# Kernel tuning notes

Hardware: AMD Instinct MI355X
Metric: run time of the kernel (lower is better)

Reference implementation:

```python
import jax, jax.numpy as jnp
import numpy as np

B, N, X, Y, W1, W2, D = 2, 6, 8, 8, 8, 8, 128
H, DH = 4, 32
L = X * Y          # number of windows
QT = N * W1 * W2   # tokens per window
EPS = 1e-5


def _ln(x, g, b):
    m = x.mean(-1, keepdims=True)
    v = ((x - m) ** 2).mean(-1, keepdims=True)
    return (x - m) * jax.lax.rsqrt(v + EPS) * g + b


def _win(t):
    # b n x y w1 w2 d -> b (x y) (n w1 w2) d
    return t.transpose(0, 2, 3, 1, 4, 5, 6).reshape(B, L, QT, D)


def setup_inputs() -> dict:
    key = jax.random.key(0)
    ks = jax.random.split(key, 12)
    s = 0.02
    inp = {
        'q': jax.random.normal(ks[0], (B, N, X, Y, W1, W2, D), jnp.float32),
        'k': jax.random.normal(ks[1], (B, N, X, Y, W1, W2, D), jnp.float32),
        'v': jax.random.normal(ks[2], (B, N, X, Y, W1, W2, D), jnp.float32),
        'skip': jax.random.normal(ks[3], (B, X, Y, W1, W2, D), jnp.float32),
        'gq': jnp.ones((D,), jnp.float32), 'betq': jnp.zeros((D,), jnp.float32),
        'gk': jnp.ones((D,), jnp.float32), 'betk': jnp.zeros((D,), jnp.float32),
        'gv': jnp.ones((D,), jnp.float32), 'betv': jnp.zeros((D,), jnp.float32),
        'wq': jax.random.normal(ks[4], (D, H * DH), jnp.float32) * s,
        'bq': jnp.zeros((H * DH,), jnp.float32),
        'wk': jax.random.normal(ks[5], (D, H * DH), jnp.float32) * s,
        'bk': jnp.zeros((H * DH,), jnp.float32),
        'wv': jax.random.normal(ks[6], (D, H * DH), jnp.float32) * s,
        'bv': jnp.zeros((H * DH,), jnp.float32),
        'wp': jax.random.normal(ks[7], (H * DH, D), jnp.float32) * s,
        'bp': jnp.zeros((D,), jnp.float32),
    }
    return inp


def reference(q, k, v, skip, gq, betq, gk, betk, gv, betv,
              wq, bq, wk, bk, wv, bv, wp, bp):
    scale = DH ** -0.5
    qw, kw, vw = _win(q), _win(k), _win(v)
    # LayerNorm + Linear QKV, split heads: (b, l, T, h, dh)
    qh = (_ln(qw, gq, betq) @ wq + bq).reshape(B, L, QT, H, DH)
    kh = (_ln(kw, gk, betk) @ wk + bk).reshape(B, L, QT, H, DH)
    vh = (_ln(vw, gv, betv) @ wv + bv).reshape(B, L, QT, H, DH)
    dot = scale * jnp.einsum('blqhd,blkhd->bhlqk', qh, kh)
    att = jax.nn.softmax(dot, axis=-1)
    a = jnp.einsum('bhlqk,blkhd->blqhd', att, vh).reshape(B, L, QT, H * DH)
    # b (x y) (n w1 w2) d -> b n x y w1 w2 d
    a = a.reshape(B, X, Y, N, W1, W2, H * DH).transpose(0, 3, 1, 2, 4, 5, 6)
    z = a @ wp + bp
    z = z.mean(1)  # average over views
    return z + skip
```

## Files before the change

kernel.cpp:

```cpp
#include <hip/hip_runtime.h>


typedef unsigned short u16;
typedef __bf16 bf16x8 __attribute__((ext_vector_type(8)));
typedef float  f32x16 __attribute__((ext_vector_type(16)));
typedef unsigned short u16x8 __attribute__((ext_vector_type(8)));

__device__ __forceinline__ u16 f2bf(float f){
  unsigned u = __float_as_uint(f);
  u += 0x7fffu + ((u >> 16) & 1u);
  return (u16)(u >> 16);
}

__device__ __forceinline__ f32x16 mfma_bf16(bf16x8 a, bf16x8 b, f32x16 c){
  return __builtin_amdgcn_mfma_f32_32x32x16_bf16(a, b, c, 0, 0, 0);
}


__global__ __launch_bounds__(128) void k_prep(
    const float* __restrict__ wq, const float* __restrict__ bq,
    const float* __restrict__ gq, const float* __restrict__ betq,
    const float* __restrict__ wk, const float* __restrict__ bk,
    const float* __restrict__ gk, const float* __restrict__ betk,
    const float* __restrict__ wv, const float* __restrict__ bv,
    const float* __restrict__ gv, const float* __restrict__ betv,
    const float* __restrict__ wp,
    u16* __restrict__ wqT, u16* __restrict__ wkT, u16* __restrict__ wvT, u16* __restrict__ wpT,
    float* __restrict__ bq2, float* __restrict__ bk2, float* __restrict__ bv2)
{
  const float ALPHA_Q = 0.17677669529663687f * 1.4426950408889634f;
  int wsel = blockIdx.x >> 2, qq = blockIdx.x & 3;
  int tid = threadIdx.x;
  const float *w, *bb, *g, *bet; u16* wT; float* b2; float alpha;
  if (wsel == 0){ w=wq; bb=bq; g=gq; bet=betq; wT=wqT; b2=bq2; alpha=ALPHA_Q; }
  else if (wsel == 1){ w=wk; bb=bk; g=gk; bet=betk; wT=wkT; b2=bk2; alpha=1.f; }
  else if (wsel == 2){ w=wv; bb=bv; g=gv; bet=betv; wT=wvT; b2=bv2; alpha=1.f; }
  else { w=wp; bb=nullptr; g=nullptr; bet=nullptr; wT=wpT; b2=nullptr; alpha=1.f; }
  float sc = (g ? g[tid] : 1.f) * alpha;
  for (int nn = 0; nn < 32; nn++){
    int n = qq*32 + nn;
    wT[n*128 + tid] = f2bf(w[tid*128 + n] * sc);
  }
  if (qq == 0 && bb){
    float s = bb[tid];
    for (int k2 = 0; k2 < 128; k2++) s += bet[k2] * w[k2*128 + tid];
    b2[tid] = s * alpha;
  }
}

__global__ __launch_bounds__(256) void k_lnproj(
    const float* __restrict__ qg, const float* __restrict__ kg, const float* __restrict__ vg,
    const u16* __restrict__ wqT, const u16* __restrict__ wkT, const u16* __restrict__ wvT,
    const float* __restrict__ bq2, const float* __restrict__ bk2, const float* __restrict__ bv2,
    u16* __restrict__ qh, u16* __restrict__ kh, u16* __restrict__ vh)
{
  __shared__ alignas(16) float Af[64*132];
  __shared__ float mean_s[64], rstd_s[64];
  __shared__ alignas(16) u16 Abf[64*136];
  int bid = blockIdx.x, tid = threadIdx.x;
  int which = bid % 3;
  int t = bid / 3;
  int n = t % 6, bl = t / 6;
  const float* src; const u16* wT; const float* b2; u16* dstb;
  if (which == 0){ src=qg; wT=wqT; b2=bq2; dstb=qh; }
  else if (which == 1){ src=kg; wT=wkT; b2=bk2; dstb=kh; }
  else { src=vg; wT=wvT; b2=bv2; dstb=vh; }
  int b = bl >> 6, l = bl & 63;
  const float4* s4 = (const float4*)(src + (size_t)((b*6 + n)*64 + l)*64*128);
  #pragma unroll
  for (int i = 0; i < 8; i++){
    int idx = tid + i*256;
    int row = idx >> 5, c4 = idx & 31;
    *(float4*)&Af[row*132 + c4*4] = s4[row*32 + c4];
  }
  __syncthreads();
  if (tid < 64){
    float s = 0.f, s2 = 0.f;
    for (int i = 0; i < 128; i++){
      int d = ((tid & 31) + i) & 127;
      float x = Af[tid*132 + d];
      s += x; s2 += x*x;
    }
    float m = s * (1.f/128.f);
    mean_s[tid] = m;
    rstd_s[tid] = rsqrtf(s2*(1.f/128.f) - m*m + 1e-5f);
  }
  __syncthreads();
  #pragma unroll
  for (int i = 0; i < 32; i++){
    int idx = tid + i*256;
    int row = idx >> 7, d = idx & 127;
    Abf[row*136 + d] = f2bf((Af[row*132 + d] - mean_s[row]) * rstd_s[row]);
  }
  __syncthreads();
  int wave = tid >> 6, lane = tid & 63, lm = lane & 31, lh = lane >> 5;
  bf16x8 bfr[8];
  const u16* wrow = wT + (32*wave + lm)*128 + lh*8;
  #pragma unroll
  for (int ks = 0; ks < 8; ks++) bfr[ks] = *(const bf16x8*)(wrow + ks*16);
  f32x16 acc0, acc1;
  #pragma unroll
  for (int r = 0; r < 16; r++){ acc0[r]=0.f; acc1[r]=0.f; }
  #pragma unroll
  for (int ks = 0; ks < 8; ks++){
    bf16x8 a0 = *(const bf16x8*)&Abf[lm*136       + ks*16 + lh*8];
    bf16x8 a1 = *(const bf16x8*)&Abf[(32+lm)*136  + ks*16 + lh*8];
    acc0 = mfma_bf16(a0, bfr[ks], acc0);
    acc1 = mfma_bf16(a1, bfr[ks], acc1);
  }
  float bias = b2[32*wave + lm];
  u16* dst = dstb + ((size_t)(bl*4 + wave)*384 + n*64)*32 + lm;
  #pragma unroll
  for (int r = 0; r < 16; r++){
    int row0 = (r&3) + 8*(r>>2) + 4*lh;
    dst[(size_t)row0*32]      = f2bf(acc0[r] + bias);
    dst[(size_t)(32+row0)*32] = f2bf(acc1[r] + bias);
  }
}

__global__ __launch_bounds__(384) void k_attn(
    const u16* __restrict__ qh, const u16* __restrict__ kh, const u16* __restrict__ vh,
    u16* __restrict__ abar)
{
  __shared__ alignas(16) u16 vts[32*392];
  __shared__ alignas(16) u16 ps[6*32*40];
  __shared__ float abar_s[64*32];
  int bid = blockIdx.x, tid = threadIdx.x;
  int h = bid & 3, bl = bid >> 2;
  const u16* qb = qh + (size_t)bid * (384*32);
  const u16* kb = kh + (size_t)bid * (384*32);
  const u16* vb = vh + (size_t)bid * (384*32);

  #pragma unroll
  for (int i = 0; i < 4; i++){
    int c = tid + i*384;
    int row = c >> 2, part = c & 3;
    u16x8 vv = *(const u16x8*)(vb + row*32 + part*8);
    #pragma unroll
    for (int j = 0; j < 8; j++) vts[(part*8 + j)*392 + row] = vv[j];
  }
  for (int idx = tid; idx < 2048; idx += 384) abar_s[idx] = 0.f;
  __syncthreads();

  int wave = tid >> 6, lane = tid & 63, lm = lane & 31, lh = lane >> 5;
  u16* pw = &ps[wave * (32*40)];

  bf16x8 qf[2][2];
  #pragma unroll
  for (int rt = 0; rt < 2; rt++)
    #pragma unroll
    for (int ks = 0; ks < 2; ks++)
      qf[rt][ks] = *(const bf16x8*)(qb + (wave*64 + rt*32 + lm)*32 + ks*16 + lh*8);

  f32x16 oacc[2];
  float lsum[32];
  #pragma unroll
  for (int r = 0; r < 16; r++){ oacc[0][r] = 0.f; oacc[1][r] = 0.f; }
  #pragma unroll
  for (int r = 0; r < 32; r++) lsum[r] = 0.f;

  for (int kt = 0; kt < 12; kt++){
    int K0 = kt*32;
    bf16x8 kf0 = *(const bf16x8*)(kb + (K0+lm)*32 +      lh*8);
    bf16x8 kf1 = *(const bf16x8*)(kb + (K0+lm)*32 + 16 + lh*8);
    bf16x8 vf0 = *(const bf16x8*)&vts[lm*392 + K0 +      lh*8];
    bf16x8 vf1 = *(const bf16x8*)&vts[lm*392 + K0 + 16 + lh*8];
    #pragma unroll
    for (int rt = 0; rt < 2; rt++){
      f32x16 s;
      #pragma unroll
      for (int r = 0; r < 16; r++) s[r] = 0.f;
      s = mfma_bf16(qf[rt][0], kf0, s);
      s = mfma_bf16(qf[rt][1], kf1, s);
      #pragma unroll
      for (int r = 0; r < 16; r++){
        float e = exp2f(s[r]);
        lsum[rt*16 + r] += e;
        pw[((r&3) + 8*(r>>2) + 4*lh)*40 + lm] = f2bf(e);
      }
      bf16x8 pf0 = *(const bf16x8*)&pw[lm*40 +      lh*8];
      bf16x8 pf1 = *(const bf16x8*)&pw[lm*40 + 16 + lh*8];
      oacc[rt] = mfma_bf16(pf0, vf0, oacc[rt]);
      oacc[rt] = mfma_bf16(pf1, vf1, oacc[rt]);
    }
  }

  #pragma unroll
  for (int rt = 0; rt < 2; rt++){
    #pragma unroll
    for (int r = 0; r < 16; r++){
      float sle = lsum[rt*16 + r];
      #pragma unroll
      for (int m = 1; m < 32; m <<= 1) sle += __shfl_xor(sle, m, 64);
      float o = oacc[rt][r] * ((1.f/6.f) / sle);
      int row0 = (r&3) + 8*(r>>2) + 4*lh;
      atomicAdd(&abar_s[(rt*32 + row0)*32 + lm], o);
    }
  }
  __syncthreads();
  u16* ob = abar + (size_t)(bl*64)*128 + h*32;
  for (int idx = tid; idx < 2048; idx += 384){
    int w12 = idx >> 5, dh = idx & 31;
    ob[(size_t)w12*128 + dh] = f2bf(abar_s[idx]);
  }
}

__global__ __launch_bounds__(256) void k_out(
    const u16* __restrict__ abar, const u16* __restrict__ wpT,
    const float* __restrict__ bp, const float* __restrict__ skip,
    float* __restrict__ out)
{
  __shared__ alignas(16) u16 Als[64*136];
  int tid = threadIdx.x;
  int R0 = blockIdx.x * 64;
  #pragma unroll
  for (int i = 0; i < 4; i++){
    int c = tid + i*256;
    int row = c >> 4, part = c & 15;
    *(u16x8*)&Als[row*136 + part*8] = *(const u16x8*)(abar + (size_t)(R0+row)*128 + part*8);
  }
  __syncthreads();
  int wave = tid >> 6, lane = tid & 63, lm = lane & 31, lh = lane >> 5;
  bf16x8 bfr[8];
  const u16* wrow = wpT + (32*wave + lm)*128 + lh*8;
  #pragma unroll
  for (int ks = 0; ks < 8; ks++) bfr[ks] = *(const bf16x8*)(wrow + ks*16);
  f32x16 acc0, acc1;
  #pragma unroll
  for (int r = 0; r < 16; r++){ acc0[r]=0.f; acc1[r]=0.f; }
  #pragma unroll
  for (int ks = 0; ks < 8; ks++){
    bf16x8 a0 = *(const bf16x8*)&Als[lm*136      + ks*16 + lh*8];
    bf16x8 a1 = *(const bf16x8*)&Als[(32+lm)*136 + ks*16 + lh*8];
    acc0 = mfma_bf16(a0, bfr[ks], acc0);
    acc1 = mfma_bf16(a1, bfr[ks], acc1);
  }
  float bias = bp[32*wave + lm];
  #pragma unroll
  for (int r = 0; r < 16; r++){
    int row0 = (r&3) + 8*(r>>2) + 4*lh;
    size_t f0 = (size_t)(R0 + row0)*128 + 32*wave + lm;
    out[f0] = acc0[r] + bias + skip[f0];
    size_t f1 = (size_t)(R0 + 32 + row0)*128 + 32*wave + lm;
    out[f1] = acc1[r] + bias + skip[f1];
  }
}

extern "C" void kernel_launch(void* const* d_in, const int* in_sizes, int n_in,
                              void* d_out, int out_size, void* d_ws, size_t ws_size,
                              hipStream_t stream)
{
  const float* q    = (const float*)d_in[0];
  const float* k    = (const float*)d_in[1];
  const float* v    = (const float*)d_in[2];
  const float* skip = (const float*)d_in[3];
  const float* gq   = (const float*)d_in[4];
  const float* betq = (const float*)d_in[5];
  const float* gk   = (const float*)d_in[6];
  const float* betk = (const float*)d_in[7];
  const float* gv   = (const float*)d_in[8];
  const float* betv = (const float*)d_in[9];
  const float* wq   = (const float*)d_in[10];
  const float* bq   = (const float*)d_in[11];
  const float* wk   = (const float*)d_in[12];
  const float* bk   = (const float*)d_in[13];
  const float* wv   = (const float*)d_in[14];
  const float* bv   = (const float*)d_in[15];
  const float* wp   = (const float*)d_in[16];
  const float* bp   = (const float*)d_in[17];
  float* out = (float*)d_out;

  char* ws = (char*)d_ws;
  u16* wqT = (u16*)ws;
  u16* wkT = wqT + 16384;
  u16* wvT = wkT + 16384;
  u16* wpT = wvT + 16384;
  float* bq2 = (float*)(ws + 131072);
  float* bk2 = bq2 + 128;
  float* bv2 = bk2 + 128;
  u16* qh = (u16*)(ws + 132608);
  u16* kh = qh + 6291456;
  u16* vh = kh + 6291456;
  u16* abar = vh + 6291456;

  k_prep  <<<16,   128, 0, stream>>>(wq,bq,gq,betq, wk,bk,gk,betk, wv,bv,gv,betv, wp,
                                     wqT,wkT,wvT,wpT, bq2,bk2,bv2);
  k_lnproj<<<2304, 256, 0, stream>>>(q,k,v, wqT,wkT,wvT, bq2,bk2,bv2, qh,kh,vh);
  k_attn  <<<512,  384, 0, stream>>>(qh,kh,vh, abar);
  k_out   <<<128,  256, 0, stream>>>(abar, wpT, bp, skip, out);
}
```

Baseline: 230.1 us.

## Fold LayerNorm into GEMM epilogue and keep softmax probabilities in registers

The LN+projection kernel now computes row sums with wave shuffles while loading, converts raw inputs straight to bf16, and applies mean/rstd after the MFMA through precomputed per-column sums of gamma-scaled weights. This removes the fp32 staging tile, one LDS pass and a barrier. The attention kernel swaps the operand order so each lane's P fragment can be fed directly into the PV MFMA, with V keys permuted in LDS to match. That drops the per-wave P round trip through shared memory, and the kernel now runs 12 waves of one 32-row tile each. Applying normalization after a bf16 GEMM on unnormalized inputs loses some precision when row means are large.

```diff
diff --git a/kernel.cpp b/kernel.cpp
--- a/kernel.cpp
+++ b/kernel.cpp
@@ -5,6 +5,9 @@
 typedef __bf16 bf16x8 __attribute__((ext_vector_type(8)));
 typedef float  f32x16 __attribute__((ext_vector_type(16)));
 typedef unsigned short u16x8 __attribute__((ext_vector_type(8)));
+typedef unsigned short u16x4 __attribute__((ext_vector_type(4)));
+
+union U8 { u16x8 u; bf16x8 b; };
 
 __device__ __forceinline__ u16 f2bf(float f){
   unsigned u = __float_as_uint(f);
@@ -26,25 +29,31 @@
     const float* __restrict__ gv, const float* __restrict__ betv,
     const float* __restrict__ wp,
     u16* __restrict__ wqT, u16* __restrict__ wkT, u16* __restrict__ wvT, u16* __restrict__ wpT,
-    float* __restrict__ bq2, float* __restrict__ bk2, float* __restrict__ bv2)
+    float* __restrict__ bq2, float* __restrict__ bk2, float* __restrict__ bv2,
+    float* __restrict__ uq2, float* __restrict__ uk2, float* __restrict__ uv2)
 {
   const float ALPHA_Q = 0.17677669529663687f * 1.4426950408889634f;
   int wsel = blockIdx.x >> 2, qq = blockIdx.x & 3;
   int tid = threadIdx.x;
-  const float *w, *bb, *g, *bet; u16* wT; float* b2; float alpha;
-  if (wsel == 0){ w=wq; bb=bq; g=gq; bet=betq; wT=wqT; b2=bq2; alpha=ALPHA_Q; }
-  else if (wsel == 1){ w=wk; bb=bk; g=gk; bet=betk; wT=wkT; b2=bk2; alpha=1.f; }
-  else if (wsel == 2){ w=wv; bb=bv; g=gv; bet=betv; wT=wvT; b2=bv2; alpha=1.f; }
-  else { w=wp; bb=nullptr; g=nullptr; bet=nullptr; wT=wpT; b2=nullptr; alpha=1.f; }
+  const float *w, *bb, *g, *bet; u16* wT; float *b2, *u2; float alpha;
+  if (wsel == 0){ w=wq; bb=bq; g=gq; bet=betq; wT=wqT; b2=bq2; u2=uq2; alpha=ALPHA_Q; }
+  else if (wsel == 1){ w=wk; bb=bk; g=gk; bet=betk; wT=wkT; b2=bk2; u2=uk2; alpha=1.f; }
+  else if (wsel == 2){ w=wv; bb=bv; g=gv; bet=betv; wT=wvT; b2=bv2; u2=uv2; alpha=1.f; }
+  else { w=wp; bb=nullptr; g=nullptr; bet=nullptr; wT=wpT; b2=nullptr; u2=nullptr; alpha=1.f; }
   float sc = (g ? g[tid] : 1.f) * alpha;
   for (int nn = 0; nn < 32; nn++){
     int n = qq*32 + nn;
     wT[n*128 + tid] = f2bf(w[tid*128 + n] * sc);
   }
   if (qq == 0 && bb){
-    float s = bb[tid];
-    for (int k2 = 0; k2 < 128; k2++) s += bet[k2] * w[k2*128 + tid];
+    float s = bb[tid], su = 0.f;
+    for (int k2 = 0; k2 < 128; k2++){
+      float wv_ = w[k2*128 + tid];
+      s  += bet[k2] * wv_;
+      su += g[k2] * wv_;
+    }
     b2[tid] = s * alpha;
+    u2[tid] = su * alpha;
   }
 }
 
@@ -52,47 +61,44 @@
     const float* __restrict__ qg, const float* __restrict__ kg, const float* __restrict__ vg,
     const u16* __restrict__ wqT, const u16* __restrict__ wkT, const u16* __restrict__ wvT,
     const float* __restrict__ bq2, const float* __restrict__ bk2, const float* __restrict__ bv2,
+    const float* __restrict__ uq2, const float* __restrict__ uk2, const float* __restrict__ uv2,
     u16* __restrict__ qh, u16* __restrict__ kh, u16* __restrict__ vh)
 {
-  __shared__ alignas(16) float Af[64*132];
-  __shared__ float mean_s[64], rstd_s[64];
   __shared__ alignas(16) u16 Abf[64*136];
+  __shared__ float s1s[64], s2s[64];
   int bid = blockIdx.x, tid = threadIdx.x;
   int which = bid % 3;
   int t = bid / 3;
   int n = t % 6, bl = t / 6;
-  const float* src; const u16* wT; const float* b2; u16* dstb;
-  if (which == 0){ src=qg; wT=wqT; b2=bq2; dstb=qh; }
-  else if (which == 1){ src=kg; wT=wkT; b2=bk2; dstb=kh; }
-  else { src=vg; wT=wvT; b2=bv2; dstb=vh; }
+  const float* src; const u16* wT; const float *b2, *u2; u16* dstb;
+  if (which == 0){ src=qg; wT=wqT; b2=bq2; u2=uq2; dstb=qh; }
+  else if (which == 1){ src=kg; wT=wkT; b2=bk2; u2=uk2; dstb=kh; }
+  else { src=vg; wT=wvT; b2=bv2; u2=uv2; dstb=vh; }
   int b = bl >> 6, l = bl & 63;
   const float4* s4 = (const float4*)(src + (size_t)((b*6 + n)*64 + l)*64*128);
   #pragma unroll
   for (int i = 0; i < 8; i++){
     int idx = tid + i*256;
     int row = idx >> 5, c4 = idx & 31;
-    *(float4*)&Af[row*132 + c4*4] = s4[row*32 + c4];
+    float4 xv = s4[idx];
+    float s1 = xv.x + xv.y + xv.z + xv.w;
+    float s2 = xv.x*xv.x + xv.y*xv.y + xv.z*xv.z + xv.w*xv.w;
+    #pragma unroll
+    for (int m = 1; m < 32; m <<= 1){
+      s1 += __shfl_xor(s1, m, 64);
+      s2 += __shfl_xor(s2, m, 64);
+    }
+    if (c4 == 0){ s1s[row] = s1; s2s[row] = s2; }
+    u16x4 pk = { f2bf(xv.x), f2bf(xv.y), f2bf(xv.z), f2bf(xv.w) };
+    *(u16x4*)&Abf[row*136 + c4*4] = pk;
   }
   __syncthreads();
   if (tid < 64){
-    float s = 0.f, s2 = 0.f;
-    for (int i = 0; i < 128; i++){
-      int d = ((tid & 31) + i) & 127;
-      float x = Af[tid*132 + d];
-      s += x; s2 += x*x;
-    }
-    float m = s * (1.f/128.f);
-    mean_s[tid] = m;
-    rstd_s[tid] = rsqrtf(s2*(1.f/128.f) - m*m + 1e-5f);
-  }
-  __syncthreads();
-  #pragma unroll
-  for (int i = 0; i < 32; i++){
-    int idx = tid + i*256;
-    int row = idx >> 7, d = idx & 127;
-    Abf[row*136 + d] = f2bf((Af[row*132 + d] - mean_s[row]) * rstd_s[row]);
-  }
-  __syncthreads();
+    float m = s1s[tid] * (1.f/128.f);
+    float r = rsqrtf(s2s[tid] * (1.f/128.f) - m*m + 1e-5f);
+    s1s[tid] = r;
+    s2s[tid] = r * m;
+  }
   int wave = tid >> 6, lane = tid & 63, lm = lane & 31, lh = lane >> 5;
   bf16x8 bfr[8];
   const u16* wrow = wT + (32*wave + lm)*128 + lh*8;
@@ -108,22 +114,25 @@
     acc0 = mfma_bf16(a0, bfr[ks], acc0);
     acc1 = mfma_bf16(a1, bfr[ks], acc1);
   }
-  float bias = b2[32*wave + lm];
+  __syncthreads();
+  int col = 32*wave + lm;
+  float u2c = u2[col], bc = b2[col];
   u16* dst = dstb + ((size_t)(bl*4 + wave)*384 + n*64)*32 + lm;
   #pragma unroll
   for (int r = 0; r < 16; r++){
     int row0 = (r&3) + 8*(r>>2) + 4*lh;
-    dst[(size_t)row0*32]      = f2bf(acc0[r] + bias);
-    dst[(size_t)(32+row0)*32] = f2bf(acc1[r] + bias);
-  }
-}
-
-__global__ __launch_bounds__(384) void k_attn(
+    float y0 = s1s[row0]     * acc0[r] - s2s[row0]     * u2c + bc;
+    float y1 = s1s[row0+32]  * acc1[r] - s2s[row0+32]  * u2c + bc;
+    dst[(size_t)row0*32]      = f2bf(y0);
+    dst[(size_t)(32+row0)*32] = f2bf(y1);
+  }
+}
+
+__global__ __launch_bounds__(768, 6) void k_attn(
     const u16* __restrict__ qh, const u16* __restrict__ kh, const u16* __restrict__ vh,
     u16* __restrict__ abar)
 {
-  __shared__ alignas(16) u16 vts[32*392];
-  __shared__ alignas(16) u16 ps[6*32*40];
+  __shared__ alignas(16) u16 vts[32*408];
   __shared__ float abar_s[64*32];
   int bid = blockIdx.x, tid = threadIdx.x;
   int h = bid & 3, bl = bid >> 2;
@@ -132,74 +141,71 @@
   const u16* vb = vh + (size_t)bid * (384*32);
 
   #pragma unroll
-  for (int i = 0; i < 4; i++){
-    int c = tid + i*384;
-    int row = c >> 2, part = c & 3;
-    u16x8 vv = *(const u16x8*)(vb + row*32 + part*8);
+  for (int i = 0; i < 2; i++){
+    int c = tid + i*768;
+    int key = c >> 2, part = c & 3;
+    int u = key & 31, tt = key >> 5;
+    int a = u >> 2;
+    int anew = (a & 4) | ((a & 1) << 1) | ((a >> 1) & 1);
+    int pos = tt*32 + anew*4 + (u & 3);
+    u16x8 vv = *(const u16x8*)(vb + key*32 + part*8);
     #pragma unroll
-    for (int j = 0; j < 8; j++) vts[(part*8 + j)*392 + row] = vv[j];
-  }
-  for (int idx = tid; idx < 2048; idx += 384) abar_s[idx] = 0.f;
+    for (int j = 0; j < 8; j++) vts[(part*8 + j)*408 + pos] = vv[j];
+  }
+  for (int idx = tid; idx < 2048; idx += 768) abar_s[idx] = 0.f;
   __syncthreads();
 
   int wave = tid >> 6, lane = tid & 63, lm = lane & 31, lh = lane >> 5;
-  u16* pw = &ps[wave * (32*40)];
-
-  bf16x8 qf[2][2];
-  #pragma unroll
-  for (int rt = 0; rt < 2; rt++)
-    #pragma unroll
-    for (int ks = 0; ks < 2; ks++)
-      qf[rt][ks] = *(const bf16x8*)(qb + (wave*64 + rt*32 + lm)*32 + ks*16 + lh*8);
-
-  f32x16 oacc[2];
-  float lsum[32];
-  #pragma unroll
-  for (int r = 0; r < 16; r++){ oacc[0][r] = 0.f; oacc[1][r] = 0.f; }
-  #pragma unroll
-  for (int r = 0; r < 32; r++) lsum[r] = 0.f;
+  int n = wave >> 1, qoff = (wave & 1) * 32;
+  int qrow = n*64 + qoff + lm;
+
+  bf16x8 qf0 = *(const bf16x8*)(qb + qrow*32 +      lh*8);
+  bf16x8 qf1 = *(const bf16x8*)(qb + qrow*32 + 16 + lh*8);
+
+  f32x16 oacc;
+  #pragma unroll
+  for (int r = 0; r < 16; r++) oacc[r] = 0.f;
+  float sle = 0.f;
+
+  const u16* vrow = &vts[lm*408 + 8*lh];
 
   for (int kt = 0; kt < 12; kt++){
     int K0 = kt*32;
     bf16x8 kf0 = *(const bf16x8*)(kb + (K0+lm)*32 +      lh*8);
     bf16x8 kf1 = *(const bf16x8*)(kb + (K0+lm)*32 + 16 + lh*8);
-    bf16x8 vf0 = *(const bf16x8*)&vts[lm*392 + K0 +      lh*8];
-    bf16x8 vf1 = *(const bf16x8*)&vts[lm*392 + K0 + 16 + lh*8];
+    f32x16 s;
     #pragma unroll
-    for (int rt = 0; rt < 2; rt++){
-      f32x16 s;
-      #pragma unroll
-      for (int r = 0; r < 16; r++) s[r] = 0.f;
-      s = mfma_bf16(qf[rt][0], kf0, s);
-      s = mfma_bf16(qf[rt][1], kf1, s);
-      #pragma unroll
-      for (int r = 0; r < 16; r++){
-        float e = exp2f(s[r]);
-        lsum[rt*16 + r] += e;
-        pw[((r&3) + 8*(r>>2) + 4*lh)*40 + lm] = f2bf(e);
-      }
-      bf16x8 pf0 = *(const bf16x8*)&pw[lm*40 +      lh*8];
-      bf16x8 pf1 = *(const bf16x8*)&pw[lm*40 + 16 + lh*8];
-      oacc[rt] = mfma_bf16(pf0, vf0, oacc[rt]);
-      oacc[rt] = mfma_bf16(pf1, vf1, oacc[rt]);
+    for (int r = 0; r < 16; r++) s[r] = 0.f;
+    s = mfma_bf16(kf0, qf0, s);
+    s = mfma_bf16(kf1, qf1, s);
+    U8 p0, p1;
+    #pragma unroll
+    for (int r = 0; r < 8; r++){
+      float e0 = exp2f(s[r]);
+      float e1 = exp2f(s[r+8]);
+      sle += e0 + e1;
+      p0.u[r] = f2bf(e0);
+      p1.u[r] = f2bf(e1);
     }
-  }
-
-  #pragma unroll
-  for (int rt = 0; rt < 2; rt++){
-    #pragma unroll
-    for (int r = 0; r < 16; r++){
-      float sle = lsum[rt*16 + r];
-      #pragma unroll
-      for (int m = 1; m < 32; m <<= 1) sle += __shfl_xor(sle, m, 64);
-      float o = oacc[rt][r] * ((1.f/6.f) / sle);
-      int row0 = (r&3) + 8*(r>>2) + 4*lh;
-      atomicAdd(&abar_s[(rt*32 + row0)*32 + lm], o);
-    }
+    U8 vb0, vb1;
+    vb0.u = *(const u16x8*)(vrow + K0);
+    vb1.u = *(const u16x8*)(vrow + K0 + 16);
+    oacc = mfma_bf16(p0.b, vb0.b, oacc);
+    oacc = mfma_bf16(p1.b, vb1.b, oacc);
+  }
+
+  sle += __shfl_xor(sle, 32, 64);
+
+  #pragma unroll
+  for (int r = 0; r < 16; r++){
+    int q_l = (r&3) + 8*(r>>2) + 4*lh;
+    float norm = __shfl(sle, q_l, 64);
+    float o = oacc[r] * ((1.f/6.f) / norm);
+    atomicAdd(&abar_s[(qoff + q_l)*32 + lm], o);
   }
   __syncthreads();
   u16* ob = abar + (size_t)(bl*64)*128 + h*32;
-  for (int idx = tid; idx < 2048; idx += 384){
+  for (int idx = tid; idx < 2048; idx += 768){
     int w12 = idx >> 5, dh = idx & 31;
     ob[(size_t)w12*128 + dh] = f2bf(abar_s[idx]);
   }
@@ -278,14 +284,17 @@
   float* bq2 = (float*)(ws + 131072);
   float* bk2 = bq2 + 128;
   float* bv2 = bk2 + 128;
-  u16* qh = (u16*)(ws + 132608);
+  float* uq2 = bv2 + 128;
+  float* uk2 = uq2 + 128;
+  float* uv2 = uk2 + 128;
+  u16* qh = (u16*)(ws + 134144);
   u16* kh = qh + 6291456;
   u16* vh = kh + 6291456;
   u16* abar = vh + 6291456;
 
   k_prep  <<<16,   128, 0, stream>>>(wq,bq,gq,betq, wk,bk,gk,betk, wv,bv,gv,betv, wp,
-                                     wqT,wkT,wvT,wpT, bq2,bk2,bv2);
-  k_lnproj<<<2304, 256, 0, stream>>>(q,k,v, wqT,wkT,wvT, bq2,bk2,bv2, qh,kh,vh);
-  k_attn  <<<512,  384, 0, stream>>>(qh,kh,vh, abar);
+                                     wqT,wkT,wvT,wpT, bq2,bk2,bv2, uq2,uk2,uv2);
+  k_lnproj<<<2304, 256, 0, stream>>>(q,k,v, wqT,wkT,wvT, bq2,bk2,bv2, uq2,uk2,uv2, qh,kh,vh);
+  k_attn  <<<512,  768, 0, stream>>>(qh,kh,vh, abar);
   k_out   <<<128,  256, 0, stream>>>(abar, wpT, bp, skip, out);
 }
```

New measurement: 224.2 us. 1.03x faster.
